# Optimization experiments

Hardware: AMD Instinct MI355X
Metric: run time of the kernel (lower is better)

The kernel has to match this reference:

```python
import jax, jax.numpy as jnp
import numpy as np

N = 8192
DIM = 128


def setup_inputs() -> dict:
    key = jax.random.key(0)
    k1, k2 = jax.random.split(key)
    mapping = jax.random.normal(k1, (N, DIM), dtype=jnp.float32)
    # Cost matrix of the finite metric: symmetric, strictly positive off-diagonal,
    # zero diagonal (the module adds eye to the denominator to handle the diagonal).
    Draw = jax.random.uniform(k2, (N, N), dtype=jnp.float32) * 2.0 + 0.1
    D = 0.5 * (Draw + Draw.T)
    D = D * (1.0 - jnp.eye(N, dtype=jnp.float32))
    return {"mapping": mapping, "D": D}


def reference(mapping, D):
    # Pairwise Euclidean distances via GEMM formulation (||a||^2 - 2ab + ||b||^2)
    # instead of materializing the O(N^2 * dim) broadcast difference.
    n = D.shape[0]
    sq = jnp.sum(mapping * mapping, axis=-1)               # [N]
    gram = mapping @ mapping.T                             # [N, N]
    d2 = sq[:, None] + sq[None, :] - 2.0 * gram            # [N, N]
    d2 = jnp.maximum(d2, 0.0)
    # safe sqrt (exact 0 on the diagonal, matching torch.norm forward)
    pos = d2 > 0
    d = jnp.sqrt(jnp.where(pos, d2, 1.0)) * pos
    ratio = jnp.abs(d - D) / (D + jnp.eye(n, dtype=D.dtype))
    return jnp.sum(ratio) / (n * n - n)
```

## Files before the change

### kernel.cpp

```cpp
#include <hip/hip_runtime.h>
#include <math.h>

#define NN 8192
#define DIM 128
#define NBLK 2048

typedef short bf16x8 __attribute__((ext_vector_type(8)));
typedef float f32x4 __attribute__((ext_vector_type(4)));

__device__ inline unsigned short f2bf(float x) {
    unsigned u = __float_as_uint(x);
    unsigned r = u + 0x7FFFu + ((u >> 16) & 1u);
    return (unsigned short)(r >> 16);
}
__device__ inline float bf2f(unsigned short h) {
    return __uint_as_float(((unsigned)h) << 16);
}

__global__ void pack_kernel(const float* __restrict__ m, unsigned short* __restrict__ buf2) {
    const int t = threadIdx.x, l = t & 63;
    const int W = blockIdx.x * 4 + (t >> 6);
    const int g = W >> 2, kq = W & 3;
    const int row = g * 16 + (l & 15);
    const int k0 = kq * 32 + (l >> 4) * 8;
    const float* src = m + (size_t)row * DIM + k0;
    float4 v0 = *reinterpret_cast<const float4*>(src);
    float4 v1 = *reinterpret_cast<const float4*>(src + 4);
    float f[8] = {v0.x, v0.y, v0.z, v0.w, v1.x, v1.y, v1.z, v1.w};
    union { ushort4 u4[2]; unsigned short us[8]; } o;
#pragma unroll
    for (int q = 0; q < 8; ++q) o.us[q] = f2bf(f[q]);
    unsigned short* dst = buf2 + (size_t)W * 512 + l * 8;
    *reinterpret_cast<ushort4*>(dst) = o.u4[0];
    *reinterpret_cast<ushort4*>(dst + 4) = o.u4[1];
}

__global__ void sq_kernel(const float* __restrict__ mapping, float* __restrict__ sq) {
    int i = blockIdx.x * blockDim.x + threadIdx.x;
    if (i < NN) {
        const float4* row = reinterpret_cast<const float4*>(mapping + (size_t)i * DIM);
        float s = 0.f;
#pragma unroll
        for (int q = 0; q < DIM / 4; ++q) {
            float4 v = row[q];
            s += v.x * v.x + v.y * v.y + v.z * v.z + v.w * v.w;
        }
        sq[i] = s;
    }
}

__global__ __launch_bounds__(512, 6) void dist_kernel(const unsigned short* __restrict__ buf2,
                                                      const float* __restrict__ D,
                                                      const float* __restrict__ sq,
                                                      float* __restrict__ partials) {
    __shared__ __align__(16) char dtile[4][64 * 144];
    __shared__ float wred[8];

    const int t = threadIdx.x, l = t & 63, w = t >> 6;
    const int b = blockIdx.x;
    const int q = b >> 4, p = b & 15;
    const int cj0 = q + p;
    float psum = 0.f;

    if (cj0 < 128) {
        const int nt = (128 - cj0 + 15) >> 4;
        const int l15 = l & 15, hi = l >> 4;
        const int colq = hi * 4;
        const int strip = w & 3;
        const int i_row = q * 64 + strip * 16 + l15;
        const int ldsoff = (strip * 16 + l15) * 144 + hi * 8;

        if (w < 4) {
            bf16x8 af[4];
#pragma unroll
            for (int kq = 0; kq < 4; ++kq)
                af[kq] = *(const bf16x8*)(buf2 + (size_t)((q * 4 + strip) * 4 + kq) * 512 + l * 8);
            const float sa = sq[i_row];

            for (int tt = 0; tt < nt; ++tt) {
                const int cj = cj0 + tt * 16;
                char* slot = &dtile[tt & 3][0];
#pragma unroll
                for (int s = 0; s < 4; ++s) {
                    bf16x8 bfr[4];
#pragma unroll
                    for (int kq = 0; kq < 4; ++kq)
                        bfr[kq] = *(const bf16x8*)(buf2 + (size_t)((cj * 4 + s) * 4 + kq) * 512 + l * 8);
                    f32x4 sb = *(const f32x4*)(sq + cj * 64 + s * 16 + colq);
                    f32x4 acc = {};
#pragma unroll
                    for (int kq = 0; kq < 4; ++kq)
                        acc = __builtin_amdgcn_mfma_f32_16x16x32_bf16(bfr[kq], af[kq], acc, 0, 0, 0);
                    ushort4 o;
                    unsigned short* op = (unsigned short*)&o;
#pragma unroll
                    for (int r = 0; r < 4; ++r) {
                        float d2 = fmaf(-2.f, acc[r], sa + sb[r]);
                        op[r] = f2bf(sqrtf(fmaxf(d2, 0.f)));
                    }
                    *reinterpret_cast<ushort4*>(slot + ldsoff + s * 32) = o;
                }
                if ((tt & 1) == 1 || tt == nt - 1) {
                    asm volatile("s_waitcnt lgkmcnt(0)" ::: "memory");
                    __builtin_amdgcn_sched_barrier(0);
                    __builtin_amdgcn_s_barrier();
                }
            }
        } else {
            const float* Drow = D + (size_t)i_row * NN;

            auto consume = [&](int tile, const f32x4(&dc)[4]) {
                const int cj = cj0 + tile * 16;
                const char* slot = &dtile[tile & 3][0];
                if (cj != q) {
#pragma unroll
                    for (int s = 0; s < 4; ++s) {
                        ushort4 o = *reinterpret_cast<const ushort4*>(slot + ldsoff + s * 32);
                        const unsigned short* op = (const unsigned short*)&o;
#pragma unroll
                        for (int r = 0; r < 4; ++r) {
                            float Dv = dc[s][r];
                            psum += __fdividef(fabsf(bf2f(op[r]) - Dv), Dv);
                        }
                    }
                } else {
#pragma unroll
                    for (int s = 0; s < 4; ++s) {
                        ushort4 o = *reinterpret_cast<const ushort4*>(slot + ldsoff + s * 32);
                        const unsigned short* op = (const unsigned short*)&o;
#pragma unroll
                        for (int r = 0; r < 4; ++r) {
                            const int j = cj * 64 + s * 16 + colq + r;
                            if (j > i_row) {
                                float Dv = dc[s][r];
                                psum += __fdividef(fabsf(bf2f(op[r]) - Dv), Dv);
                            }
                        }
                    }
                }
            };

            f32x4 dA[4], dB[4];
#pragma unroll
            for (int s = 0; s < 4; ++s)
                dA[s] = *(const f32x4*)(Drow + cj0 * 64 + s * 16 + colq);

            bool cur_a = true;
            for (int tt = 0; tt < nt; ++tt) {
                if ((tt & 1) == 0) __builtin_amdgcn_s_barrier();
                const int ncj = cj0 + (tt + 1) * 16;
                if (cur_a) {
                    if (tt + 1 < nt) {
#pragma unroll
                        for (int s = 0; s < 4; ++s)
                            dB[s] = *(const f32x4*)(Drow + ncj * 64 + s * 16 + colq);
                    }
                    consume(tt, dA);
                } else {
                    if (tt + 1 < nt) {
#pragma unroll
                        for (int s = 0; s < 4; ++s)
                            dA[s] = *(const f32x4*)(Drow + ncj * 64 + s * 16 + colq);
                    }
                    consume(tt, dB);
                }
                cur_a = !cur_a;
            }
        }
    }

    for (int off = 32; off > 0; off >>= 1) psum += __shfl_down(psum, off, 64);
    __syncthreads();
    if (l == 0) wred[w] = psum;
    __syncthreads();
    if (t == 0) {
        float s = 0.f;
#pragma unroll
        for (int k = 0; k < 8; ++k) s += wred[k];
        partials[b] = 2.f * s;
    }
}

__global__ void reduce_kernel(const float* __restrict__ partials, float* __restrict__ out) {
    __shared__ double sm[256];
    const int t = threadIdx.x;
    double s = 0.0;
    for (int i = t; i < NBLK; i += 256) s += (double)partials[i];
    sm[t] = s;
    __syncthreads();
    for (int off = 128; off > 0; off >>= 1) {
        if (t < off) sm[t] += sm[t + off];
        __syncthreads();
    }
    if (t == 0) out[0] = (float)(sm[0] / ((double)NN * (double)NN - (double)NN));
}

extern "C" void kernel_launch(void* const* d_in, const int* in_sizes, int n_in,
                              void* d_out, int out_size, void* d_ws, size_t ws_size,
                              hipStream_t stream) {
    const float* mapping = (const float*)d_in[0];
    const float* D       = (const float*)d_in[1];
    float* out = (float*)d_out;

    unsigned short* buf2 = (unsigned short*)d_ws;
    float* sq            = (float*)(buf2 + NN * DIM);
    float* partials      = sq + NN;

    pack_kernel<<<512, 256, 0, stream>>>(mapping, buf2);
    sq_kernel<<<NN / 256, 256, 0, stream>>>(mapping, sq);
    dist_kernel<<<NBLK, 512, 0, stream>>>(buf2, D, sq, partials);
    reduce_kernel<<<1, 256, 0, stream>>>(partials, out);
}
```

Baseline: 68.57 us.

## Retile distance kernel to 32x256 tiles with row-contiguous coalesced D loads

The tile shape changes from 64 rows by 64 columns to 32 rows by 256 columns. Consumer waves now read whole contiguous 1KB row segments of D, one per row, so the bandwidth-bound D stream is better coalesced. The block and tile schedule is remapped to 8 column phases per row block, and launch bounds are lowered from 6 to 4 waves per SIMD to allow more registers for the eight-deep prefetch. In exchange, occupancy drops and the block-level load balance changes.

```diff
diff --git a/kernel.cpp b/kernel.cpp
--- a/kernel.cpp
+++ b/kernel.cpp
@@ -49,44 +49,43 @@
     }
 }
 
-__global__ __launch_bounds__(512, 6) void dist_kernel(const unsigned short* __restrict__ buf2,
+__global__ __launch_bounds__(512, 4) void dist_kernel(const unsigned short* __restrict__ buf2,
                                                       const float* __restrict__ D,
                                                       const float* __restrict__ sq,
                                                       float* __restrict__ partials) {
-    __shared__ __align__(16) char dtile[4][64 * 144];
+    __shared__ __align__(16) unsigned short dts[4][32][264];
     __shared__ float wred[8];
 
     const int t = threadIdx.x, l = t & 63, w = t >> 6;
     const int b = blockIdx.x;
-    const int q = b >> 4, p = b & 15;
-    const int cj0 = q + p;
+    const int q = b >> 3, p = b & 7;
+    const int c0 = (q >> 3) + p;
     float psum = 0.f;
 
-    if (cj0 < 128) {
-        const int nt = (128 - cj0 + 15) >> 4;
+    if (c0 < 32) {
+        const int nt = ((31 - c0) >> 3) + 1;
         const int l15 = l & 15, hi = l >> 4;
-        const int colq = hi * 4;
-        const int strip = w & 3;
-        const int i_row = q * 64 + strip * 16 + l15;
-        const int ldsoff = (strip * 16 + l15) * 144 + hi * 8;
 
         if (w < 4) {
+            const int rg = w & 1, sh = (w >> 1) * 8;
+            const int i_row = q * 32 + rg * 16 + l15;
             bf16x8 af[4];
 #pragma unroll
             for (int kq = 0; kq < 4; ++kq)
-                af[kq] = *(const bf16x8*)(buf2 + (size_t)((q * 4 + strip) * 4 + kq) * 512 + l * 8);
+                af[kq] = *(const bf16x8*)(buf2 + (size_t)((q * 2 + rg) * 4 + kq) * 512 + l * 8);
             const float sa = sq[i_row];
 
             for (int tt = 0; tt < nt; ++tt) {
-                const int cj = cj0 + tt * 16;
-                char* slot = &dtile[tt & 3][0];
-#pragma unroll
-                for (int s = 0; s < 4; ++s) {
+                const int c = c0 + tt * 8;
+                unsigned short (*slot)[264] = dts[tt & 3];
+#pragma unroll
+                for (int s2 = 0; s2 < 8; ++s2) {
+                    const int s = sh + s2;
                     bf16x8 bfr[4];
 #pragma unroll
                     for (int kq = 0; kq < 4; ++kq)
-                        bfr[kq] = *(const bf16x8*)(buf2 + (size_t)((cj * 4 + s) * 4 + kq) * 512 + l * 8);
-                    f32x4 sb = *(const f32x4*)(sq + cj * 64 + s * 16 + colq);
+                        bfr[kq] = *(const bf16x8*)(buf2 + (size_t)((c * 16 + s) * 4 + kq) * 512 + l * 8);
+                    f32x4 sb = *(const f32x4*)(sq + c * 256 + s * 16 + hi * 4);
                     f32x4 acc = {};
 #pragma unroll
                     for (int kq = 0; kq < 4; ++kq)
@@ -98,7 +97,7 @@
                         float d2 = fmaf(-2.f, acc[r], sa + sb[r]);
                         op[r] = f2bf(sqrtf(fmaxf(d2, 0.f)));
                     }
-                    *reinterpret_cast<ushort4*>(slot + ldsoff + s * 32) = o;
+                    *reinterpret_cast<ushort4*>(&slot[rg * 16 + l15][s * 16 + hi * 4]) = o;
                 }
                 if ((tt & 1) == 1 || tt == nt - 1) {
                     asm volatile("s_waitcnt lgkmcnt(0)" ::: "memory");
@@ -107,60 +106,65 @@
                 }
             }
         } else {
-            const float* Drow = D + (size_t)i_row * NN;
-
-            auto consume = [&](int tile, const f32x4(&dc)[4]) {
-                const int cj = cj0 + tile * 16;
-                const char* slot = &dtile[tile & 3][0];
-                if (cj != q) {
-#pragma unroll
-                    for (int s = 0; s < 4; ++s) {
-                        ushort4 o = *reinterpret_cast<const ushort4*>(slot + ldsoff + s * 32);
-                        const unsigned short* op = (const unsigned short*)&o;
+            const int cw = w - 4;
+            const int row0 = cw * 8;
+            const size_t Dbase = (size_t)(q * 32 + row0) * NN + l * 4;
+            const int cdiag = q >> 3;
+
+            f32x4 dA[8], dB[8];
+
+            auto consume = [&](int tt, const f32x4(&dd)[8]) {
+                const int c = c0 + tt * 8;
+                const unsigned short (*slot)[264] = dts[tt & 3];
+                if (c != cdiag) {
+#pragma unroll
+                    for (int k = 0; k < 8; ++k) {
+                        ushort4 dv = *reinterpret_cast<const ushort4*>(&slot[row0 + k][l * 4]);
+                        const unsigned short* dp = (const unsigned short*)&dv;
 #pragma unroll
                         for (int r = 0; r < 4; ++r) {
-                            float Dv = dc[s][r];
-                            psum += __fdividef(fabsf(bf2f(op[r]) - Dv), Dv);
+                            float Dv = dd[k][r];
+                            psum += __fdividef(fabsf(bf2f(dp[r]) - Dv), Dv);
                         }
                     }
                 } else {
 #pragma unroll
-                    for (int s = 0; s < 4; ++s) {
-                        ushort4 o = *reinterpret_cast<const ushort4*>(slot + ldsoff + s * 32);
-                        const unsigned short* op = (const unsigned short*)&o;
+                    for (int k = 0; k < 8; ++k) {
+                        const int i_g = q * 32 + row0 + k;
+                        ushort4 dv = *reinterpret_cast<const ushort4*>(&slot[row0 + k][l * 4]);
+                        const unsigned short* dp = (const unsigned short*)&dv;
 #pragma unroll
                         for (int r = 0; r < 4; ++r) {
-                            const int j = cj * 64 + s * 16 + colq + r;
-                            if (j > i_row) {
-                                float Dv = dc[s][r];
-                                psum += __fdividef(fabsf(bf2f(op[r]) - Dv), Dv);
+                            const int j = c * 256 + l * 4 + r;
+                            if (j > i_g) {
+                                float Dv = dd[k][r];
+                                psum += __fdividef(fabsf(bf2f(dp[r]) - Dv), Dv);
                             }
                         }
                     }
                 }
             };
 
-            f32x4 dA[4], dB[4];
-#pragma unroll
-            for (int s = 0; s < 4; ++s)
-                dA[s] = *(const f32x4*)(Drow + cj0 * 64 + s * 16 + colq);
+#pragma unroll
+            for (int k = 0; k < 8; ++k)
+                dA[k] = *(const f32x4*)(D + Dbase + (size_t)k * NN + c0 * 256);
 
             bool cur_a = true;
             for (int tt = 0; tt < nt; ++tt) {
                 if ((tt & 1) == 0) __builtin_amdgcn_s_barrier();
-                const int ncj = cj0 + (tt + 1) * 16;
+                const int cn = c0 + (tt + 1) * 8;
                 if (cur_a) {
                     if (tt + 1 < nt) {
 #pragma unroll
-                        for (int s = 0; s < 4; ++s)
-                            dB[s] = *(const f32x4*)(Drow + ncj * 64 + s * 16 + colq);
+                        for (int k = 0; k < 8; ++k)
+                            dB[k] = *(const f32x4*)(D + Dbase + (size_t)k * NN + cn * 256);
                     }
                     consume(tt, dA);
                 } else {
                     if (tt + 1 < nt) {
 #pragma unroll
-                        for (int s = 0; s < 4; ++s)
-                            dA[s] = *(const f32x4*)(Drow + ncj * 64 + s * 16 + colq);
+                        for (int k = 0; k < 8; ++k)
+                            dA[k] = *(const f32x4*)(D + Dbase + (size_t)k * NN + cn * 256);
                     }
                     consume(tt, dB);
                 }
```

After: 84.59 us. 23.4% more time.
